# Kernel optimization log

Hardware: AMD Instinct MI355X
Metric: run time of the kernel (lower is better)

The kernel has to match this reference:

```python
import jax, jax.numpy as jnp
import numpy as np

EMBED_DIM = 1024
NUM_HEADS = 16
HEAD_DIM = EMBED_DIM // NUM_HEADS


def setup_inputs() -> dict:
    key = jax.random.key(0)
    ks = jax.random.split(key, 9)
    B, S, E, hd = 2, 2048, EMBED_DIM, HEAD_DIM
    s_e = 1.0 / np.sqrt(E)
    return {
        "x": jax.random.normal(ks[0], (B, S, E), dtype=jnp.float32),
        "wq": jax.random.uniform(ks[1], (E, E), jnp.float32, -s_e, s_e),
        "bq": jax.random.uniform(ks[2], (E,), jnp.float32, -s_e, s_e),
        "wk": jax.random.uniform(ks[3], (E, hd), jnp.float32, -s_e, s_e),
        "bk": jax.random.uniform(ks[4], (hd,), jnp.float32, -s_e, s_e),
        "wv": jax.random.uniform(ks[5], (E, hd), jnp.float32, -s_e, s_e),
        "bv": jax.random.uniform(ks[6], (hd,), jnp.float32, -s_e, s_e),
        "wo": jax.random.uniform(ks[7], (E, E), jnp.float32, -s_e, s_e),
        "bo": jax.random.uniform(ks[8], (E,), jnp.float32, -s_e, s_e),
    }


def reference(x, wq, bq, wk, bk, wv, bv, wo, bo):
    B, S, E = x.shape
    H, hd = NUM_HEADS, HEAD_DIM
    # projections
    q = (x @ wq + bq).reshape(B, S, H, hd)          # [B,S,H,hd]
    k = x @ wk + bk                                  # [B,S,hd] shared across heads
    v = x @ wv + bv                                  # [B,S,hd]
    scale = 1.0 / np.sqrt(hd).astype(np.float32)
    # scores: [B,H,S_q,S_k]
    scores = jnp.einsum('bqhd,bkd->bhqk', q, k) * scale
    attn = jax.nn.softmax(scores, axis=-1)
    out = jnp.einsum('bhqk,bkd->bqhd', attn, v).reshape(B, S, E)
    return out @ wo + bo
```

## Files before the change

### kernel.cpp

```cpp
#include <hip/hip_runtime.h>
#include <stdint.h>

#define SLEN 2048
#define EDIM 1024
#define NH 16
#define HD 64
#define QLD 1152
#define PLD 136

typedef unsigned short u16;
typedef short bf8 __attribute__((ext_vector_type(8)));
typedef float f4 __attribute__((ext_vector_type(4)));
typedef bf8 bf8_a __attribute__((may_alias));
typedef uint2 uint2_a __attribute__((may_alias));
typedef uint4 uint4_a __attribute__((may_alias));

__device__ __forceinline__ float bf2f(u16 u) {
  union { unsigned u; float f; } c; c.u = ((unsigned)u) << 16; return c.f;
}
__device__ __forceinline__ u16 f2bf(float x) {
  union { float f; unsigned u; } c; c.f = x;
  return (u16)((c.u + 0x7FFFu + ((c.u >> 16) & 1u)) >> 16);
}
__device__ __forceinline__ void async_cp16(u16* lds, const u16* g) {
  __builtin_amdgcn_global_load_lds((__attribute__((address_space(1))) void*)g,
                                   (__attribute__((address_space(3))) void*)lds,
                                   16, 0, 0);
}

__global__ void probe_dtype(const unsigned* __restrict__ x, int* __restrict__ flag) {
  __shared__ int red[256];
  const int t = threadIdx.x;
  int cnt = 0;
  for (int i = t; i < 1024; i += 256) {
    unsigned e = (x[i] >> 7) & 0xFFu;
    cnt += (e >= 0x70u && e <= 0x8Fu) ? 1 : 0;
  }
  red[t] = cnt;
  __syncthreads();
  for (int s = 128; s > 0; s >>= 1) {
    if (t < s) red[t] += red[t + s];
    __syncthreads();
  }
  if (t == 0) *flag = (red[0] >= 512) ? 1 : 0;
}

__global__ void convert_x(const void* __restrict__ src, u16* __restrict__ dst,
                          const int* __restrict__ flag) {
  const int i = (blockIdx.x * 256 + threadIdx.x) * 8;
  if (*flag) {
    *(uint4_a*)&dst[i] = *(const uint4_a*)((const u16*)src + i);
  } else {
    const float* s = (const float*)src;
    u16 tmp[8];
#pragma unroll
    for (int j = 0; j < 8; ++j) tmp[j] = f2bf(s[i + j]);
    *(uint4_a*)&dst[i] = *(const uint4_a*)tmp;
  }
}

__device__ __forceinline__ void tcvt_tile(const void* src, int srcLd,
                                          u16* dst, int dstLd, int r0, int c0,
                                          bool isbf) {
  __shared__ u16 tile[64][65];
  const int t = threadIdx.x;
#pragma unroll
  for (int i = 0; i < 16; ++i) {
    int e = i * 256 + t, rr = e >> 6, cc = e & 63;
    size_t idx = (size_t)(r0 + rr) * srcLd + c0 + cc;
    tile[rr][cc] = isbf ? ((const u16*)src)[idx] : f2bf(((const float*)src)[idx]);
  }
  __syncthreads();
#pragma unroll
  for (int i = 0; i < 16; ++i) {
    int e = i * 256 + t, j = e >> 6, ii = e & 63;
    dst[(size_t)(c0 + j) * dstLd + r0 + ii] = tile[ii][j];
  }
}

__global__ void tcvt_qo(const void* wq, u16* wT, const void* wo, u16* woT,
                        const int* __restrict__ flag) {
  const bool isbf = (*flag != 0);
  const int yy = blockIdx.y;
  if (yy < 16) tcvt_tile(wq, 1024, wT, 1024, blockIdx.x * 64, yy * 64, isbf);
  else         tcvt_tile(wo, 1024, woT, 1024, blockIdx.x * 64, (yy - 16) * 64, isbf);
}
__global__ void tcvt_kv(const void* wk, const void* wv, u16* wT,
                        const int* __restrict__ flag) {
  const bool isbf = (*flag != 0);
  if (blockIdx.y == 0)
    tcvt_tile(wk, 64, wT + (size_t)1024 * 1024, 1024, blockIdx.x * 64, 0, isbf);
  else
    tcvt_tile(wv, 64, wT + (size_t)1088 * 1024, 1024, blockIdx.x * 64, 0, isbf);
}

__global__ void tpose_v(const u16* __restrict__ qkvb, u16* __restrict__ vTb) {
  __shared__ u16 tile[64][65];
  const int b = blockIdx.y, r0 = blockIdx.x * 64;
  const u16* src = qkvb + (size_t)b * SLEN * QLD + 1088;
  u16* dst = vTb + (size_t)b * 64 * SLEN;
  const int t = threadIdx.x;
#pragma unroll
  for (int i = 0; i < 16; ++i) {
    int e = i * 256 + t, rr = e >> 6, cc = e & 63;
    tile[rr][cc] = src[(size_t)(r0 + rr) * QLD + cc];
  }
  __syncthreads();
#pragma unroll
  for (int i = 0; i < 16; ++i) {
    int e = i * 256 + t, j = e >> 6, ii = e & 63;
    dst[(size_t)j * SLEN + r0 + ii] = tile[ii][j];
  }
}

__global__ void prep_bias(const void* bq, const void* bk, const void* bv,
                          const void* bo, float* biasQKV, float* biasOut,
                          const int* __restrict__ flag) {
  const bool isbf = (*flag != 0);
  int i = blockIdx.x * 256 + threadIdx.x;
  auto rd = [&](const void* p, int idx) -> float {
    return isbf ? bf2f(((const u16*)p)[idx]) : ((const float*)p)[idx];
  };
  if (i < 1024) biasQKV[i] = rd(bq, i);
  else if (i < 1088) biasQKV[i] = rd(bk, i - 1024);
  else if (i < 1152) biasQKV[i] = rd(bv, i - 1088);
  int j = i - 1152;
  if (j >= 0 && j < 1024) biasOut[j] = rd(bo, j);
}

__global__ __launch_bounds__(256) void gemm_bt_bias(
    const u16* __restrict__ A, const u16* __restrict__ Bt,
    const float* __restrict__ bias, void* __restrict__ C, int K, int ldc,
    int ofp32) {
  __shared__ __align__(16) u16 As[64 * 64];
  __shared__ __align__(16) u16 Bs[128 * 64];
  const int tn0 = blockIdx.x * 128, tm0 = blockIdx.y * 64;
  const int tid = threadIdx.x, wave = tid >> 6, lane = tid & 63;
  const int quad = lane >> 4, l16 = lane & 15;
  const int wm = wave & 1, wn = wave >> 1;

  f4 acc[2][4];
#pragma unroll
  for (int i = 0; i < 2; ++i)
#pragma unroll
    for (int j = 0; j < 4; ++j) acc[i][j] = f4{0.f, 0.f, 0.f, 0.f};

  int aslot[2], bslot[4]; size_t aoff[2], boff[4];
#pragma unroll
  for (int i = 0; i < 2; ++i) {
    int s = i * 256 + tid, m = s >> 3, kc = s & 7, c = (kc - m) & 7;
    aslot[i] = s; aoff[i] = (size_t)(tm0 + m) * K + c * 8;
  }
#pragma unroll
  for (int i = 0; i < 4; ++i) {
    int s = i * 256 + tid, n = s >> 3, kc = s & 7, c = (kc - n) & 7;
    bslot[i] = s; boff[i] = (size_t)(tn0 + n) * K + c * 8;
  }
  int ard[2][2], brd[4][2];
#pragma unroll
  for (int mi = 0; mi < 2; ++mi) {
    int m = wm * 32 + mi * 16 + l16;
#pragma unroll
    for (int kk = 0; kk < 2; ++kk)
      ard[mi][kk] = (m * 8 + (((kk * 4 + quad) + m) & 7)) * 8;
  }
#pragma unroll
  for (int ni = 0; ni < 4; ++ni) {
    int n = wn * 64 + ni * 16 + l16;
#pragma unroll
    for (int kk = 0; kk < 2; ++kk)
      brd[ni][kk] = (n * 8 + (((kk * 4 + quad) + n) & 7)) * 8;
  }

  const int kIt = K >> 6;
  for (int it = 0; it < kIt; ++it) {
    __syncthreads();
    const size_t kb = (size_t)it * 64;
#pragma unroll
    for (int i = 0; i < 2; ++i) async_cp16(&As[aslot[i] * 8], A + aoff[i] + kb);
#pragma unroll
    for (int i = 0; i < 4; ++i) async_cp16(&Bs[bslot[i] * 8], Bt + boff[i] + kb);
    __syncthreads();
#pragma unroll
    for (int kk = 0; kk < 2; ++kk) {
      bf8 af[2], bfr[4];
#pragma unroll
      for (int mi = 0; mi < 2; ++mi) af[mi] = *(const bf8_a*)&As[ard[mi][kk]];
#pragma unroll
      for (int ni = 0; ni < 4; ++ni) bfr[ni] = *(const bf8_a*)&Bs[brd[ni][kk]];
#pragma unroll
      for (int mi = 0; mi < 2; ++mi)
#pragma unroll
        for (int ni = 0; ni < 4; ++ni)
          acc[mi][ni] = __builtin_amdgcn_mfma_f32_16x16x32_bf16(
              af[mi], bfr[ni], acc[mi][ni], 0, 0, 0);
    }
  }

  float bv[4];
#pragma unroll
  for (int ni = 0; ni < 4; ++ni) bv[ni] = bias[tn0 + wn * 64 + ni * 16 + l16];
#pragma unroll
  for (int mi = 0; mi < 2; ++mi) {
    int row0 = tm0 + wm * 32 + mi * 16 + quad * 4;
#pragma unroll
    for (int ni = 0; ni < 4; ++ni) {
      int col = tn0 + wn * 64 + ni * 16 + l16;
#pragma unroll
      for (int r = 0; r < 4; ++r) {
        float v = acc[mi][ni][r] + bv[ni];
        if (ofp32) ((float*)C)[(size_t)(row0 + r) * ldc + col] = v;
        else       ((u16*)C)[(size_t)(row0 + r) * ldc + col] = f2bf(v);
      }
    }
  }
}

__global__ __launch_bounds__(512, 4) void attn_kernel(
    const u16* __restrict__ qkv, const u16* __restrict__ vT,
    u16* __restrict__ aout) {
  __shared__ __align__(16) u16 Kf[8192];
  __shared__ __align__(16) u16 Vf[8192];
  __shared__ __align__(16) u16 Ps[128 * PLD];
  const int qt = blockIdx.x, bh = blockIdx.y, b = bh >> 4, h = bh & 15;
  const int tid = threadIdx.x, wave = tid >> 6, lane = tid & 63;
  const int quad = lane >> 4, l16 = lane & 15;

#pragma unroll
  for (int i = 0; i < 2; ++i) {
    int d = i * 512 + tid;
    int kk = d >> 9, w8 = (d >> 6) & 7, qd = (d >> 4) & 3, r16 = d & 15;
    async_cp16(&Kf[d * 8],
               qkv + (size_t)(b * SLEN + qt * 128 + w8 * 16 + r16) * QLD +
                   h * HD + (kk * 4 + qd) * 8);
  }
  __syncthreads();
  bf8 bq[2];
#pragma unroll
  for (int kk = 0; kk < 2; ++kk)
    bq[kk] = *(const bf8_a*)&Kf[((kk * 8 + wave) * 64 + lane) * 8];

  f4 acc_o[4];
#pragma unroll
  for (int j = 0; j < 4; ++j) acc_o[j] = f4{0.f, 0.f, 0.f, 0.f};
  float l_run = 0.f;
  const float C1 = 0.125f * 1.44269504089f;
  const int prow = (wave * 16 + l16) * PLD;

  for (int kt = 0; kt < 16; ++kt) {
    __syncthreads();
#pragma unroll
    for (int i = 0; i < 2; ++i) {
      int d = i * 512 + tid;
      int kk = d >> 9, k8 = (d >> 6) & 7, qd = (d >> 4) & 3, r16 = d & 15;
      async_cp16(&Kf[d * 8],
                 qkv + (size_t)(b * SLEN + kt * 128 + k8 * 16 + r16) * QLD +
                     EDIM + (kk * 4 + qd) * 8);
    }
#pragma unroll
    for (int i = 0; i < 2; ++i) {
      int d = i * 512 + tid;
      int k4 = d >> 8, ni = (d >> 6) & 3, qd = (d >> 4) & 3, r16 = d & 15;
      async_cp16(&Vf[d * 8],
                 vT + (size_t)(b * 64 + ni * 16 + r16) * SLEN + kt * 128 +
                     (k4 * 4 + qd) * 8);
    }
    __syncthreads();

    f4 st[8];
#pragma unroll
    for (int k8 = 0; k8 < 8; ++k8) st[k8] = f4{0.f, 0.f, 0.f, 0.f};
#pragma unroll
    for (int kk = 0; kk < 2; ++kk)
#pragma unroll
      for (int k8 = 0; k8 < 8; ++k8) {
        bf8 ak = *(const bf8_a*)&Kf[((kk * 8 + k8) * 64 + lane) * 8];
        st[k8] = __builtin_amdgcn_mfma_f32_16x16x32_bf16(ak, bq[kk], st[k8], 0, 0, 0);
      }

    float rs = 0.f;
#pragma unroll
    for (int k8 = 0; k8 < 8; ++k8) {
      float p0 = __builtin_amdgcn_exp2f(st[k8][0] * C1);
      float p1 = __builtin_amdgcn_exp2f(st[k8][1] * C1);
      float p2 = __builtin_amdgcn_exp2f(st[k8][2] * C1);
      float p3 = __builtin_amdgcn_exp2f(st[k8][3] * C1);
      rs += (p0 + p1) + (p2 + p3);
      uint2 pk;
      pk.x = (unsigned)f2bf(p0) | ((unsigned)f2bf(p1) << 16);
      pk.y = (unsigned)f2bf(p2) | ((unsigned)f2bf(p3) << 16);
      *(uint2_a*)&Ps[prow + k8 * 16 + quad * 4] = pk;
    }
    rs += __shfl_xor(rs, 16, 64);
    rs += __shfl_xor(rs, 32, 64);
    l_run += rs;
    __syncthreads();

#pragma unroll
    for (int k4 = 0; k4 < 4; ++k4) {
      bf8 ap = *(const bf8_a*)&Ps[prow + k4 * 32 + quad * 8];
#pragma unroll
      for (int ni = 0; ni < 4; ++ni) {
        bf8 bv = *(const bf8_a*)&Vf[((k4 * 4 + ni) * 64 + lane) * 8];
        acc_o[ni] = __builtin_amdgcn_mfma_f32_16x16x32_bf16(ap, bv, acc_o[ni], 0, 0, 0);
      }
    }
  }

#pragma unroll
  for (int r = 0; r < 4; ++r) {
    float li = __shfl(l_run, quad * 4 + r, 64);
    float inv = 1.f / li;
    size_t row = (size_t)(b * SLEN + qt * 128 + wave * 16 + quad * 4 + r);
#pragma unroll
    for (int ni = 0; ni < 4; ++ni)
      aout[row * EDIM + h * HD + ni * 16 + l16] = f2bf(acc_o[ni][r] * inv);
  }
}

extern "C" void kernel_launch(void* const* d_in, const int* in_sizes, int n_in,
                              void* d_out, int out_size, void* d_ws, size_t ws_size,
                              hipStream_t stream) {
  const void* x  = d_in[0];
  const void* wq = d_in[1];
  const void* bq = d_in[2];
  const void* wk = d_in[3];
  const void* bk = d_in[4];
  const void* wv = d_in[5];
  const void* bv = d_in[6];
  const void* wo = d_in[7];
  const void* bo = d_in[8];

  char* ws = (char*)d_ws;
  size_t off = 0;
  auto carve = [&](size_t bytes) {
    void* p = ws + off;
    off = (off + bytes + 255) & ~(size_t)255;
    return p;
  };
  int* dflag   = (int*)carve(256);
  u16* xbf     = (u16*)carve((size_t)4096 * EDIM * 2);
  u16* wT      = (u16*)carve((size_t)1152 * 1024 * 2);
  u16* woT     = (u16*)carve((size_t)1024 * 1024 * 2);
  float* bQKV  = (float*)carve(1152 * 4);
  float* bOut  = (float*)carve(1024 * 4);
  u16* qkvb    = (u16*)carve((size_t)4096 * QLD * 2);
  u16* vTb     = (u16*)carve((size_t)2 * 64 * SLEN * 2);
  u16* aob     = (u16*)carve((size_t)4096 * EDIM * 2);

  probe_dtype<<<dim3(1), 256, 0, stream>>>((const unsigned*)x, dflag);
  convert_x<<<dim3(2048), 256, 0, stream>>>(x, xbf, dflag);
  tcvt_qo<<<dim3(16, 32), 256, 0, stream>>>(wq, wT, wo, woT, dflag);
  tcvt_kv<<<dim3(16, 2), 256, 0, stream>>>(wk, wv, wT, dflag);
  prep_bias<<<dim3(9), 256, 0, stream>>>(bq, bk, bv, bo, bQKV, bOut, dflag);

  gemm_bt_bias<<<dim3(9, 64), 256, 0, stream>>>(xbf, wT, bQKV, qkvb, 1024, QLD, 0);

  tpose_v<<<dim3(32, 2), 256, 0, stream>>>(qkvb, vTb);

  attn_kernel<<<dim3(16, 32), 512, 0, stream>>>(qkvb, vTb, aob);

  gemm_bt_bias<<<dim3(8, 64), 256, 0, stream>>>(aob, woT, bOut, d_out, 1024, 1024, 1);
}
```

Before: 202.9 us.

## Enlarge GEMM tiles to 128x128 and give attention waves two query tiles

The projection GEMM tile grows from 64x128 to 128x128, so each wave computes a 4x4 grid of MFMA tiles. This raises data reuse per LDS load but halves the grid to 288 and 256 blocks. The attention kernel goes from 512 to 256 threads, with each wave handling 32 query rows in two 16-row tiles, so K and V fragments read from LDS are reused across both. The P buffer is relaid out in fragment order so it can be read back with conflict-free vector loads. bf16 conversion now uses hardware casts with packed pairs. The cost is more registers per thread and fewer blocks, which may hurt occupancy.

```diff
diff --git a/kernel.cpp b/kernel.cpp
--- a/kernel.cpp
+++ b/kernel.cpp
@@ -6,7 +6,6 @@
 #define NH 16
 #define HD 64
 #define QLD 1152
-#define PLD 136
 
 typedef unsigned short u16;
 typedef short bf8 __attribute__((ext_vector_type(8)));
@@ -19,8 +18,12 @@
   union { unsigned u; float f; } c; c.u = ((unsigned)u) << 16; return c.f;
 }
 __device__ __forceinline__ u16 f2bf(float x) {
-  union { float f; unsigned u; } c; c.f = x;
-  return (u16)((c.u + 0x7FFFu + ((c.u >> 16) & 1u)) >> 16);
+  union { __bf16 h; u16 u; } c; c.h = (__bf16)x; return c.u;
+}
+__device__ __forceinline__ unsigned pk2bf(float a, float b) {
+  union { __bf16 h[2]; unsigned u; } c;
+  c.h[0] = (__bf16)a; c.h[1] = (__bf16)b;
+  return c.u;
 }
 __device__ __forceinline__ void async_cp16(u16* lds, const u16* g) {
   __builtin_amdgcn_global_load_lds((__attribute__((address_space(1))) void*)g,
@@ -132,34 +135,31 @@
     const u16* __restrict__ A, const u16* __restrict__ Bt,
     const float* __restrict__ bias, void* __restrict__ C, int K, int ldc,
     int ofp32) {
-  __shared__ __align__(16) u16 As[64 * 64];
+  __shared__ __align__(16) u16 As[128 * 64];
   __shared__ __align__(16) u16 Bs[128 * 64];
-  const int tn0 = blockIdx.x * 128, tm0 = blockIdx.y * 64;
+  const int tn0 = blockIdx.x * 128, tm0 = blockIdx.y * 128;
   const int tid = threadIdx.x, wave = tid >> 6, lane = tid & 63;
   const int quad = lane >> 4, l16 = lane & 15;
   const int wm = wave & 1, wn = wave >> 1;
 
-  f4 acc[2][4];
-#pragma unroll
-  for (int i = 0; i < 2; ++i)
+  f4 acc[4][4];
+#pragma unroll
+  for (int i = 0; i < 4; ++i)
 #pragma unroll
     for (int j = 0; j < 4; ++j) acc[i][j] = f4{0.f, 0.f, 0.f, 0.f};
 
-  int aslot[2], bslot[4]; size_t aoff[2], boff[4];
-#pragma unroll
-  for (int i = 0; i < 2; ++i) {
+  int slot[4]; size_t aoff[4], boff[4];
+#pragma unroll
+  for (int i = 0; i < 4; ++i) {
     int s = i * 256 + tid, m = s >> 3, kc = s & 7, c = (kc - m) & 7;
-    aslot[i] = s; aoff[i] = (size_t)(tm0 + m) * K + c * 8;
-  }
-#pragma unroll
-  for (int i = 0; i < 4; ++i) {
-    int s = i * 256 + tid, n = s >> 3, kc = s & 7, c = (kc - n) & 7;
-    bslot[i] = s; boff[i] = (size_t)(tn0 + n) * K + c * 8;
-  }
-  int ard[2][2], brd[4][2];
-#pragma unroll
-  for (int mi = 0; mi < 2; ++mi) {
-    int m = wm * 32 + mi * 16 + l16;
+    slot[i] = s;
+    aoff[i] = (size_t)(tm0 + m) * K + c * 8;
+    boff[i] = (size_t)(tn0 + m) * K + c * 8;
+  }
+  int ard[4][2], brd[4][2];
+#pragma unroll
+  for (int mi = 0; mi < 4; ++mi) {
+    int m = wm * 64 + mi * 16 + l16;
 #pragma unroll
     for (int kk = 0; kk < 2; ++kk)
       ard[mi][kk] = (m * 8 + (((kk * 4 + quad) + m) & 7)) * 8;
@@ -177,19 +177,20 @@
     __syncthreads();
     const size_t kb = (size_t)it * 64;
 #pragma unroll
-    for (int i = 0; i < 2; ++i) async_cp16(&As[aslot[i] * 8], A + aoff[i] + kb);
-#pragma unroll
-    for (int i = 0; i < 4; ++i) async_cp16(&Bs[bslot[i] * 8], Bt + boff[i] + kb);
+    for (int i = 0; i < 4; ++i) {
+      async_cp16(&As[slot[i] * 8], A + aoff[i] + kb);
+      async_cp16(&Bs[slot[i] * 8], Bt + boff[i] + kb);
+    }
     __syncthreads();
 #pragma unroll
     for (int kk = 0; kk < 2; ++kk) {
-      bf8 af[2], bfr[4];
-#pragma unroll
-      for (int mi = 0; mi < 2; ++mi) af[mi] = *(const bf8_a*)&As[ard[mi][kk]];
+      bf8 af[4], bfr[4];
+#pragma unroll
+      for (int mi = 0; mi < 4; ++mi) af[mi] = *(const bf8_a*)&As[ard[mi][kk]];
 #pragma unroll
       for (int ni = 0; ni < 4; ++ni) bfr[ni] = *(const bf8_a*)&Bs[brd[ni][kk]];
 #pragma unroll
-      for (int mi = 0; mi < 2; ++mi)
+      for (int mi = 0; mi < 4; ++mi)
 #pragma unroll
         for (int ni = 0; ni < 4; ++ni)
           acc[mi][ni] = __builtin_amdgcn_mfma_f32_16x16x32_bf16(
@@ -201,8 +202,8 @@
 #pragma unroll
   for (int ni = 0; ni < 4; ++ni) bv[ni] = bias[tn0 + wn * 64 + ni * 16 + l16];
 #pragma unroll
-  for (int mi = 0; mi < 2; ++mi) {
-    int row0 = tm0 + wm * 32 + mi * 16 + quad * 4;
+  for (int mi = 0; mi < 4; ++mi) {
+    int row0 = tm0 + wm * 64 + mi * 16 + quad * 4;
 #pragma unroll
     for (int ni = 0; ni < 4; ++ni) {
       int col = tn0 + wn * 64 + ni * 16 + l16;
@@ -216,50 +217,53 @@
   }
 }
 
-__global__ __launch_bounds__(512, 4) void attn_kernel(
+__global__ __launch_bounds__(256, 2) void attn_kernel(
     const u16* __restrict__ qkv, const u16* __restrict__ vT,
     u16* __restrict__ aout) {
   __shared__ __align__(16) u16 Kf[8192];
   __shared__ __align__(16) u16 Vf[8192];
-  __shared__ __align__(16) u16 Ps[128 * PLD];
+  __shared__ __align__(16) u16 Ps[16384];
   const int qt = blockIdx.x, bh = blockIdx.y, b = bh >> 4, h = bh & 15;
   const int tid = threadIdx.x, wave = tid >> 6, lane = tid & 63;
   const int quad = lane >> 4, l16 = lane & 15;
 
 #pragma unroll
-  for (int i = 0; i < 2; ++i) {
-    int d = i * 512 + tid;
-    int kk = d >> 9, w8 = (d >> 6) & 7, qd = (d >> 4) & 3, r16 = d & 15;
+  for (int i = 0; i < 4; ++i) {
+    int d = i * 256 + tid;
+    int kk = d >> 9, g = (d >> 6) & 7, qd = (d >> 4) & 3, r16 = d & 15;
     async_cp16(&Kf[d * 8],
-               qkv + (size_t)(b * SLEN + qt * 128 + w8 * 16 + r16) * QLD +
+               qkv + (size_t)(b * SLEN + qt * 128 + g * 16 + r16) * QLD +
                    h * HD + (kk * 4 + qd) * 8);
   }
   __syncthreads();
-  bf8 bq[2];
-#pragma unroll
-  for (int kk = 0; kk < 2; ++kk)
-    bq[kk] = *(const bf8_a*)&Kf[((kk * 8 + wave) * 64 + lane) * 8];
-
-  f4 acc_o[4];
-#pragma unroll
-  for (int j = 0; j < 4; ++j) acc_o[j] = f4{0.f, 0.f, 0.f, 0.f};
-  float l_run = 0.f;
+  bf8 bq[2][2];
+#pragma unroll
+  for (int nt = 0; nt < 2; ++nt)
+#pragma unroll
+    for (int kk = 0; kk < 2; ++kk)
+      bq[nt][kk] = *(const bf8_a*)&Kf[((kk * 8 + wave * 2 + nt) * 64 + lane) * 8];
+
+  f4 acc_o[2][4];
+#pragma unroll
+  for (int i = 0; i < 2; ++i)
+#pragma unroll
+    for (int j = 0; j < 4; ++j) acc_o[i][j] = f4{0.f, 0.f, 0.f, 0.f};
+  f4 lr4[2] = {f4{0.f, 0.f, 0.f, 0.f}, f4{0.f, 0.f, 0.f, 0.f}};
   const float C1 = 0.125f * 1.44269504089f;
-  const int prow = (wave * 16 + l16) * PLD;
 
   for (int kt = 0; kt < 16; ++kt) {
     __syncthreads();
 #pragma unroll
-    for (int i = 0; i < 2; ++i) {
-      int d = i * 512 + tid;
+    for (int i = 0; i < 4; ++i) {
+      int d = i * 256 + tid;
       int kk = d >> 9, k8 = (d >> 6) & 7, qd = (d >> 4) & 3, r16 = d & 15;
       async_cp16(&Kf[d * 8],
                  qkv + (size_t)(b * SLEN + kt * 128 + k8 * 16 + r16) * QLD +
                      EDIM + (kk * 4 + qd) * 8);
     }
 #pragma unroll
-    for (int i = 0; i < 2; ++i) {
-      int d = i * 512 + tid;
+    for (int i = 0; i < 4; ++i) {
+      int d = i * 256 + tid;
       int k4 = d >> 8, ni = (d >> 6) & 3, qd = (d >> 4) & 3, r16 = d & 15;
       async_cp16(&Vf[d * 8],
                  vT + (size_t)(b * 64 + ni * 16 + r16) * SLEN + kt * 128 +
@@ -267,55 +271,74 @@
     }
     __syncthreads();
 
-    f4 st[8];
-#pragma unroll
-    for (int k8 = 0; k8 < 8; ++k8) st[k8] = f4{0.f, 0.f, 0.f, 0.f};
+    f4 st[8][2];
+#pragma unroll
+    for (int k8 = 0; k8 < 8; ++k8)
+#pragma unroll
+      for (int nt = 0; nt < 2; ++nt) st[k8][nt] = f4{0.f, 0.f, 0.f, 0.f};
 #pragma unroll
     for (int kk = 0; kk < 2; ++kk)
 #pragma unroll
       for (int k8 = 0; k8 < 8; ++k8) {
         bf8 ak = *(const bf8_a*)&Kf[((kk * 8 + k8) * 64 + lane) * 8];
-        st[k8] = __builtin_amdgcn_mfma_f32_16x16x32_bf16(ak, bq[kk], st[k8], 0, 0, 0);
+#pragma unroll
+        for (int nt = 0; nt < 2; ++nt)
+          st[k8][nt] = __builtin_amdgcn_mfma_f32_16x16x32_bf16(ak, bq[nt][kk], st[k8][nt], 0, 0, 0);
       }
 
-    float rs = 0.f;
-#pragma unroll
-    for (int k8 = 0; k8 < 8; ++k8) {
-      float p0 = __builtin_amdgcn_exp2f(st[k8][0] * C1);
-      float p1 = __builtin_amdgcn_exp2f(st[k8][1] * C1);
-      float p2 = __builtin_amdgcn_exp2f(st[k8][2] * C1);
-      float p3 = __builtin_amdgcn_exp2f(st[k8][3] * C1);
-      rs += (p0 + p1) + (p2 + p3);
-      uint2 pk;
-      pk.x = (unsigned)f2bf(p0) | ((unsigned)f2bf(p1) << 16);
-      pk.y = (unsigned)f2bf(p2) | ((unsigned)f2bf(p3) << 16);
-      *(uint2_a*)&Ps[prow + k8 * 16 + quad * 4] = pk;
-    }
-    rs += __shfl_xor(rs, 16, 64);
-    rs += __shfl_xor(rs, 32, 64);
-    l_run += rs;
+#pragma unroll
+    for (int nt = 0; nt < 2; ++nt)
+#pragma unroll
+      for (int k8 = 0; k8 < 8; ++k8) {
+        f4 pe;
+        pe[0] = __builtin_amdgcn_exp2f(st[k8][nt][0] * C1);
+        pe[1] = __builtin_amdgcn_exp2f(st[k8][nt][1] * C1);
+        pe[2] = __builtin_amdgcn_exp2f(st[k8][nt][2] * C1);
+        pe[3] = __builtin_amdgcn_exp2f(st[k8][nt][3] * C1);
+        lr4[nt] += pe;
+        uint2 pk;
+        pk.x = pk2bf(pe[0], pe[1]);
+        pk.y = pk2bf(pe[2], pe[3]);
+        int c = nt * 256 + (k8 >> 1) * 64 + (((k8 << 1) + (quad >> 1)) & 3) * 16 + l16;
+        *(uint2_a*)&Ps[(wave * 512 + c) * 8 + (quad & 1) * 4] = pk;
+      }
     __syncthreads();
 
 #pragma unroll
     for (int k4 = 0; k4 < 4; ++k4) {
-      bf8 ap = *(const bf8_a*)&Ps[prow + k4 * 32 + quad * 8];
+      bf8 ap[2];
+#pragma unroll
+      for (int mt = 0; mt < 2; ++mt)
+        ap[mt] = *(const bf8_a*)&Ps[(wave * 512 + mt * 256 + k4 * 64 + quad * 16 + l16) * 8];
 #pragma unroll
       for (int ni = 0; ni < 4; ++ni) {
         bf8 bv = *(const bf8_a*)&Vf[((k4 * 4 + ni) * 64 + lane) * 8];
-        acc_o[ni] = __builtin_amdgcn_mfma_f32_16x16x32_bf16(ap, bv, acc_o[ni], 0, 0, 0);
+#pragma unroll
+        for (int mt = 0; mt < 2; ++mt)
+          acc_o[mt][ni] = __builtin_amdgcn_mfma_f32_16x16x32_bf16(ap[mt], bv, acc_o[mt][ni], 0, 0, 0);
       }
     }
   }
 
-#pragma unroll
-  for (int r = 0; r < 4; ++r) {
-    float li = __shfl(l_run, quad * 4 + r, 64);
-    float inv = 1.f / li;
-    size_t row = (size_t)(b * SLEN + qt * 128 + wave * 16 + quad * 4 + r);
-#pragma unroll
-    for (int ni = 0; ni < 4; ++ni)
-      aout[row * EDIM + h * HD + ni * 16 + l16] = f2bf(acc_o[ni][r] * inv);
-  }
+  float ls[2];
+#pragma unroll
+  for (int nt = 0; nt < 2; ++nt) {
+    float s = (lr4[nt][0] + lr4[nt][1]) + (lr4[nt][2] + lr4[nt][3]);
+    s += __shfl_xor(s, 16, 64);
+    s += __shfl_xor(s, 32, 64);
+    ls[nt] = s;
+  }
+#pragma unroll
+  for (int mt = 0; mt < 2; ++mt)
+#pragma unroll
+    for (int r = 0; r < 4; ++r) {
+      float li = __shfl(ls[mt], quad * 4 + r, 64);
+      float inv = 1.f / li;
+      size_t row = (size_t)(b * SLEN + qt * 128 + wave * 32 + mt * 16 + quad * 4 + r);
+#pragma unroll
+      for (int ni = 0; ni < 4; ++ni)
+        aout[row * EDIM + h * HD + ni * 16 + l16] = f2bf(acc_o[mt][ni][r] * inv);
+    }
 }
 
 extern "C" void kernel_launch(void* const* d_in, const int* in_sizes, int n_in,
@@ -354,11 +377,11 @@
   tcvt_kv<<<dim3(16, 2), 256, 0, stream>>>(wk, wv, wT, dflag);
   prep_bias<<<dim3(9), 256, 0, stream>>>(bq, bk, bv, bo, bQKV, bOut, dflag);
 
-  gemm_bt_bias<<<dim3(9, 64), 256, 0, stream>>>(xbf, wT, bQKV, qkvb, 1024, QLD, 0);
+  gemm_bt_bias<<<dim3(9, 32), 256, 0, stream>>>(xbf, wT, bQKV, qkvb, 1024, QLD, 0);
 
   tpose_v<<<dim3(32, 2), 256, 0, stream>>>(qkvb, vTb);
 
-  attn_kernel<<<dim3(16, 32), 512, 0, stream>>>(qkvb, vTb, aob);
-
-  gemm_bt_bias<<<dim3(8, 64), 256, 0, stream>>>(aob, woT, bOut, d_out, 1024, 1024, 1);
-}
+  attn_kernel<<<dim3(16, 32), 256, 0, stream>>>(qkvb, vTb, aob);
+
+  gemm_bt_bias<<<dim3(8, 32), 256, 0, stream>>>(aob, woT, bOut, d_out, 1024, 1024, 1);
+}
```

Result: slower. 210.5 us (+3.7%).
